# Kernel optimization log

Hardware: AMD Instinct MI355X
Metric: run time of the kernel (lower is better)

## Reference

```python
import jax, jax.numpy as jnp
import numpy as np

D_MODEL, JOINT_DIM, VOCAB = 512, 640, 1024
B, T, U = 4, 256, 64


def setup_inputs() -> dict:
    key = jax.random.key(0)
    ks = jax.random.split(key, 8)
    s_in = 1.0 / np.sqrt(D_MODEL)
    s_j = 1.0 / np.sqrt(JOINT_DIM)
    return {
        "enc": jax.random.normal(ks[0], (B, T, D_MODEL), jnp.float32),
        "pred": jax.random.normal(ks[1], (B, U, D_MODEL), jnp.float32),
        "enc_w": jax.random.uniform(ks[2], (JOINT_DIM, D_MODEL), jnp.float32, -s_in, s_in),
        "enc_b": jax.random.uniform(ks[3], (JOINT_DIM,), jnp.float32, -s_in, s_in),
        "pred_w": jax.random.uniform(ks[4], (JOINT_DIM, D_MODEL), jnp.float32, -s_in, s_in),
        "pred_b": jax.random.uniform(ks[5], (JOINT_DIM,), jnp.float32, -s_in, s_in),
        "out_w": jax.random.uniform(ks[6], (VOCAB, JOINT_DIM), jnp.float32, -s_j, s_j),
        "out_b": jax.random.uniform(ks[7], (VOCAB,), jnp.float32, -s_j, s_j),
    }


def reference(enc, pred, enc_w, enc_b, pred_w, pred_b, out_w, out_b):
    # project encoder (B,T,J) and predictor (B,U,J)
    e = jnp.einsum("btd,jd->btj", enc, enc_w) + enc_b
    p = jnp.einsum("bud,jd->buj", pred, pred_w) + pred_b
    # broadcast add over the (T,U) grid, tanh, then vocab projection
    z = jnp.tanh(e[:, :, None, :] + p[:, None, :, :])  # (B,T,U,J)
    logits = jnp.einsum("btuj,vj->btuv", z, out_w) + out_b  # (B,T,U,V)
    return logits
```

## Files before the change

kernel.cpp:

```cpp
#include <hip/hip_runtime.h>
#include <cstdint>
#include <cstddef>


typedef __attribute__((ext_vector_type(8))) __bf16 bf16x8;
typedef __attribute__((ext_vector_type(4))) float f32x4;

__device__ __forceinline__ int swz(int row, int kElem) {
  return (row << 6) + (kElem ^ ((row & 7) << 3));
}

__device__ __forceinline__ float fast_tanh(float x) {
  float e = __builtin_amdgcn_exp2f(x * 2.88539008177793f);
  return 1.0f - 2.0f * __builtin_amdgcn_rcpf(e + 1.0f);
}

__device__ __forceinline__ void gload_lds16(const void* g, void* l) {
  __builtin_amdgcn_global_load_lds(
      (const __attribute__((address_space(1))) void*)g,
      (__attribute__((address_space(3))) void*)l, 16, 0, 0);
}

__device__ void proj_tile(const float* __restrict__ A, const float* __restrict__ W,
                          const float* __restrict__ bias, __bf16* __restrict__ C,
                          int mt, int nt, __bf16* As, __bf16* Bs)
{
  const int tid  = threadIdx.x;
  const int r = tid & 127, half = tid >> 7;
  const int lane = tid & 63, wv = tid >> 6;
  const int wm = wv >> 1, wn = wv & 1;

  const float* arow = A + (size_t)(mt * 128 + r) * 512 + half * 32;
  const float* wrow = W + (size_t)(nt * 128 + r) * 512 + half * 32;

  f32x4 acc[4][4] = {};

  for (int k0 = 0; k0 < 512; k0 += 64) {
#pragma unroll
    for (int s = 0; s < 4; ++s) {
      f32x4 a0 = *(const f32x4*)(arow + k0 + s * 8);
      f32x4 a1 = *(const f32x4*)(arow + k0 + s * 8 + 4);
      f32x4 w0 = *(const f32x4*)(wrow + k0 + s * 8);
      f32x4 w1 = *(const f32x4*)(wrow + k0 + s * 8 + 4);
      bf16x8 za, zw;
#pragma unroll
      for (int j = 0; j < 4; ++j) {
        za[j] = (__bf16)a0[j]; za[4 + j] = (__bf16)a1[j];
        zw[j] = (__bf16)w0[j]; zw[4 + j] = (__bf16)w1[j];
      }
      const int kk = half * 32 + s * 8;
      *(bf16x8*)&As[swz(r, kk)] = za;
      *(bf16x8*)&Bs[swz(r, kk)] = zw;
    }
    __syncthreads();
#pragma unroll
    for (int kk = 0; kk < 2; ++kk) {
      bf16x8 af[4], bfr[4];
#pragma unroll
      for (int i = 0; i < 4; ++i) {
        af[i]  = *(const bf16x8*)&As[swz(wm * 64 + i * 16 + (lane & 15), kk * 32 + (lane >> 4) * 8)];
        bfr[i] = *(const bf16x8*)&Bs[swz(wn * 64 + i * 16 + (lane & 15), kk * 32 + (lane >> 4) * 8)];
      }
#pragma unroll
      for (int mi = 0; mi < 4; ++mi)
#pragma unroll
        for (int ni = 0; ni < 4; ++ni)
          acc[mi][ni] = __builtin_amdgcn_mfma_f32_16x16x32_bf16(af[mi], bfr[ni], acc[mi][ni], 0, 0, 0);
    }
    __syncthreads();
  }

  const int rowbase = mt * 128 + wm * 64;
  const int colbase = nt * 128 + wn * 64;
#pragma unroll
  for (int ni = 0; ni < 4; ++ni) {
    const int col = colbase + ni * 16 + (lane & 15);
    const float bb = bias[col];
#pragma unroll
    for (int mi = 0; mi < 4; ++mi) {
      const int row = rowbase + mi * 16 + (lane >> 4) * 4;
#pragma unroll
      for (int rg = 0; rg < 4; ++rg)
        C[(size_t)(row + rg) * 640 + col] = (__bf16)(acc[mi][ni][rg] + bb);
    }
  }
}

__global__ __launch_bounds__(256) void prep_kernel(
    const float* __restrict__ enc,  const float* __restrict__ enc_w,  const float* __restrict__ enc_b,
    const float* __restrict__ pred, const float* __restrict__ pred_w, const float* __restrict__ pred_b,
    const float* __restrict__ out_w,
    __bf16* __restrict__ E, __bf16* __restrict__ P, __bf16* __restrict__ Wb)
{
  __shared__ __align__(16) __bf16 As[128 * 64];
  __shared__ __align__(16) __bf16 Bs[128 * 64];
  const int bid = blockIdx.x;
  if (bid < 40) {
    proj_tile(enc, enc_w, enc_b, E, bid / 5, bid % 5, As, Bs);
  } else if (bid < 50) {
    proj_tile(pred, pred_w, pred_b, P, (bid - 40) / 5, (bid - 40) % 5, As, Bs);
  } else {
    const int gid = (bid - 50) * 256 + threadIdx.x;
    const int v  = gid / 80;
    const int j8 = gid % 80;
    f32x4 w0 = *(const f32x4*)(out_w + (size_t)v * 640 + j8 * 8);
    f32x4 w1 = *(const f32x4*)(out_w + (size_t)v * 640 + j8 * 8 + 4);
    bf16x8 z;
#pragma unroll
    for (int j = 0; j < 4; ++j) { z[j] = (__bf16)w0[j]; z[4 + j] = (__bf16)w1[j]; }
    const int nb = v >> 8, rr = v & 255;
    const int kb = j8 >> 3, kk = (j8 & 7) * 8;
    *(bf16x8*)(Wb + ((size_t)(nb * 10 + kb) << 14) + swz(rr, kk)) = z;
  }
}

__global__ __launch_bounds__(512, 4) void joiner_main(
    const __bf16* __restrict__ E, const __bf16* __restrict__ P,
    const __bf16* __restrict__ Wb, const float* __restrict__ outb,
    float* __restrict__ out)
{
  __shared__ __align__(16) __bf16 As[8192];
  __shared__ __align__(16) __bf16 Bs[2][16384];
  const int tid = threadIdx.x;
  const int nt = blockIdx.x & 3;
  const int mt = blockIdx.x >> 2;
  const int row0 = mt << 7;
  const int b  = row0 >> 14;
  const int t0 = (row0 >> 6) & 255;
  const int ar = tid & 127, h = tid >> 7;
  const int lane = tid & 63, wv = tid >> 6;
  const int wm = wv >> 2, wn = wv & 3;

  const __bf16* ep = E + (size_t)((b << 8) + t0 + (ar >> 6)) * 640 + h * 16;
  const __bf16* pp = P + (size_t)((b << 6) + (ar & 63)) * 640 + h * 16;
  const __bf16* wsrc = Wb + ((size_t)(nt * 10) << 14);

  f32x4 acc[4][4] = {};
  bf16x8 eA[2], pA[2];

  auto stageB = [&](int kt, __bf16* dst) {
#pragma unroll
    for (int c = 0; c < 4; ++c)
      gload_lds16(wsrc + ((size_t)kt << 14) + c * 4096 + wv * 512 + lane * 8,
                  dst + c * 4096 + wv * 512);
  };
  auto loadEP = [&](int k0) {
#pragma unroll
    for (int c = 0; c < 2; ++c) {
      eA[c] = *(const bf16x8*)(ep + k0 + c * 8);
      pA[c] = *(const bf16x8*)(pp + k0 + c * 8);
    }
  };
  auto writeA = [&]() {
#pragma unroll
    for (int c = 0; c < 2; ++c) {
      bf16x8 z;
#pragma unroll
      for (int j = 0; j < 8; ++j)
        z[j] = (__bf16)fast_tanh((float)eA[c][j] + (float)pA[c][j]);
      *(bf16x8*)&As[swz(ar, h * 16 + c * 8)] = z;
    }
  };
  auto compute = [&](const __bf16* Bsc) {
#pragma unroll
    for (int kk = 0; kk < 2; ++kk) {
      bf16x8 af[4], bfr[4];
#pragma unroll
      for (int i = 0; i < 4; ++i) {
        af[i]  = *(const bf16x8*)&As[swz(wm * 64 + i * 16 + (lane & 15), kk * 32 + (lane >> 4) * 8)];
        bfr[i] = *(const bf16x8*)&Bsc[swz(wn * 64 + i * 16 + (lane & 15), kk * 32 + (lane >> 4) * 8)];
      }
      asm volatile("s_waitcnt lgkmcnt(0)" ::: "memory");
      __builtin_amdgcn_sched_barrier(0);
      __builtin_amdgcn_s_setprio(1);
#pragma unroll
      for (int mi = 0; mi < 4; ++mi)
#pragma unroll
        for (int ni = 0; ni < 4; ++ni)
          acc[mi][ni] = __builtin_amdgcn_mfma_f32_16x16x32_bf16(af[mi], bfr[ni], acc[mi][ni], 0, 0, 0);
      __builtin_amdgcn_s_setprio(0);
    }
  };

  stageB(0, Bs[0]);
  loadEP(0);
  writeA();
  asm volatile("s_waitcnt vmcnt(0) lgkmcnt(0)" ::: "memory");
  __builtin_amdgcn_s_barrier();

  for (int kt = 0; kt < 9; ++kt) {
    const int cur = kt & 1;
    stageB(kt + 1, Bs[cur ^ 1]);
    loadEP((kt + 1) << 6);
    compute(Bs[cur]);
    __builtin_amdgcn_s_barrier();
    __builtin_amdgcn_sched_barrier(0);
    writeA();
    asm volatile("s_waitcnt lgkmcnt(0)" ::: "memory");
    __builtin_amdgcn_s_barrier();
  }
  compute(Bs[1]);

  const int rowbase = row0 + wm * 64;
  const int colbase = (nt << 8) + wn * 64;
#pragma unroll
  for (int ni = 0; ni < 4; ++ni) {
    const int col = colbase + ni * 16 + (lane & 15);
    const float bb = outb[col];
#pragma unroll
    for (int mi = 0; mi < 4; ++mi) {
      const int row = rowbase + mi * 16 + (lane >> 4) * 4;
#pragma unroll
      for (int rg = 0; rg < 4; ++rg)
        out[(size_t)(row + rg) * 1024 + col] = acc[mi][ni][rg] + bb;
    }
  }
}

extern "C" void kernel_launch(void* const* d_in, const int* in_sizes, int n_in,
                              void* d_out, int out_size, void* d_ws, size_t ws_size,
                              hipStream_t stream) {
  const float* enc    = (const float*)d_in[0];
  const float* pred   = (const float*)d_in[1];
  const float* enc_w  = (const float*)d_in[2];
  const float* enc_b  = (const float*)d_in[3];
  const float* pred_w = (const float*)d_in[4];
  const float* pred_b = (const float*)d_in[5];
  const float* out_w  = (const float*)d_in[6];
  const float* out_b  = (const float*)d_in[7];
  float* out = (float*)d_out;

  char* ws = (char*)d_ws;
  __bf16* E  = (__bf16*)(ws);
  __bf16* P  = (__bf16*)(ws + 1310720);
  __bf16* Wb = (__bf16*)(ws + 1638400);

  prep_kernel<<<dim3(370), dim3(256), 0, stream>>>(
      enc, enc_w, enc_b, pred, pred_w, pred_b, out_w, E, P, Wb);
  joiner_main<<<dim3(2048), dim3(512), 0, stream>>>(E, P, Wb, out_b, out);
}
```

Measured before the change: 172.8 us.

## Materialize tanh joint tensor then run plain tiled GEMM, fallback to fused

```diff
diff --git a/kernel.cpp b/kernel.cpp
--- a/kernel.cpp
+++ b/kernel.cpp
@@ -108,13 +108,102 @@
     bf16x8 z;
 #pragma unroll
     for (int j = 0; j < 4; ++j) { z[j] = (__bf16)w0[j]; z[4 + j] = (__bf16)w1[j]; }
-    const int nb = v >> 8, rr = v & 255;
+    const int nb = v >> 7, rr = v & 127;
     const int kb = j8 >> 3, kk = (j8 & 7) * 8;
-    *(bf16x8*)(Wb + ((size_t)(nb * 10 + kb) << 14) + swz(rr, kk)) = z;
-  }
-}
-
-__global__ __launch_bounds__(512, 4) void joiner_main(
+    *(bf16x8*)(Wb + ((size_t)(nb * 10 + kb) << 13) + swz(rr, kk)) = z;
+  }
+}
+
+__global__ __launch_bounds__(256) void zprod_kernel(
+    const __bf16* __restrict__ E, const __bf16* __restrict__ P,
+    __bf16* __restrict__ Z)
+{
+  const int bid = blockIdx.x;
+  const int mt = bid / 10, kt = bid % 10;
+  const int row0 = mt << 7;
+  const int b  = row0 >> 14;
+  const int t0 = (row0 >> 6) & 255;
+  __bf16* zdst = Z + ((size_t)bid << 13);
+  const int k0 = kt << 6;
+
+#pragma unroll
+  for (int c = 0; c < 4; ++c) {
+    const int o = c * 2048 + threadIdx.x * 8;
+    const int r = o >> 6;
+    const int k = (o & 63) ^ ((r & 7) << 3);
+    const __bf16* ep = E + (size_t)((b << 8) + t0 + (r >> 6)) * 640 + k0 + k;
+    const __bf16* pp = P + (size_t)((b << 6) + (r & 63)) * 640 + k0 + k;
+    bf16x8 e8 = *(const bf16x8*)ep;
+    bf16x8 p8 = *(const bf16x8*)pp;
+    bf16x8 z;
+#pragma unroll
+    for (int j = 0; j < 8; ++j)
+      z[j] = (__bf16)fast_tanh((float)e8[j] + (float)p8[j]);
+    *(bf16x8*)&zdst[o] = z;
+  }
+}
+
+__global__ __launch_bounds__(256) void joiner_mainz(
+    const __bf16* __restrict__ Z, const __bf16* __restrict__ Wb,
+    const float* __restrict__ outb, float* __restrict__ out)
+{
+  __shared__ __align__(16) __bf16 As[8192];
+  __shared__ __align__(16) __bf16 Bs[8192];
+  const int wg = blockIdx.x;
+  const int bid = (wg & 7) * 512 + (wg >> 3);
+  const int mt = bid >> 3, nt = bid & 7;
+  const int tid = threadIdx.x;
+  const int lane = tid & 63, wv = tid >> 6;
+  const int wm = wv >> 1, wn = wv & 1;
+
+  const __bf16* zsrc = Z  + ((size_t)(mt * 10) << 13);
+  const __bf16* wsrc = Wb + ((size_t)(nt * 10) << 13);
+
+  f32x4 acc[4][4] = {};
+
+  for (int kt = 0; kt < 10; ++kt) {
+    const size_t kb = (size_t)kt << 13;
+#pragma unroll
+    for (int c = 0; c < 4; ++c) {
+      const int off = c * 2048 + wv * 512;
+      gload_lds16(zsrc + kb + off + lane * 8, &As[off]);
+      gload_lds16(wsrc + kb + off + lane * 8, &Bs[off]);
+    }
+    __syncthreads();
+#pragma unroll
+    for (int kk = 0; kk < 2; ++kk) {
+      bf16x8 af[4], bfr[4];
+#pragma unroll
+      for (int i = 0; i < 4; ++i) {
+        af[i]  = *(const bf16x8*)&As[swz(wm * 64 + i * 16 + (lane & 15), kk * 32 + (lane >> 4) * 8)];
+        bfr[i] = *(const bf16x8*)&Bs[swz(wn * 64 + i * 16 + (lane & 15), kk * 32 + (lane >> 4) * 8)];
+      }
+#pragma unroll
+      for (int mi = 0; mi < 4; ++mi)
+#pragma unroll
+        for (int ni = 0; ni < 4; ++ni)
+          acc[mi][ni] = __builtin_amdgcn_mfma_f32_16x16x32_bf16(af[mi], bfr[ni], acc[mi][ni], 0, 0, 0);
+    }
+    __syncthreads();
+  }
+
+  const int rowbase = (mt << 7) + wm * 64;
+  const int colbase = (nt << 7) + wn * 64;
+#pragma unroll
+  for (int ni = 0; ni < 4; ++ni) {
+    const int col = colbase + ni * 16 + (lane & 15);
+    const float bb = outb[col];
+#pragma unroll
+    for (int mi = 0; mi < 4; ++mi) {
+      const int row = rowbase + mi * 16 + (lane >> 4) * 4;
+#pragma unroll
+      for (int rg = 0; rg < 4; ++rg)
+        out[(size_t)(row + rg) * 1024 + col] = acc[mi][ni][rg] + bb;
+    }
+  }
+}
+
+__global__ __launch_bounds__(512, 4) void joiner_fused(
     const __bf16* __restrict__ E, const __bf16* __restrict__ P,
     const __bf16* __restrict__ Wb, const float* __restrict__ outb,
     float* __restrict__ out)
@@ -133,16 +222,29 @@
 
   const __bf16* ep = E + (size_t)((b << 8) + t0 + (ar >> 6)) * 640 + h * 16;
   const __bf16* pp = P + (size_t)((b << 6) + (ar & 63)) * 640 + h * 16;
-  const __bf16* wsrc = Wb + ((size_t)(nt * 10) << 14);
 
   f32x4 acc[4][4] = {};
   bf16x8 eA[2], pA[2];
 
   auto stageB = [&](int kt, __bf16* dst) {
 #pragma unroll
-    for (int c = 0; c < 4; ++c)
-      gload_lds16(wsrc + ((size_t)kt << 14) + c * 4096 + wv * 512 + lane * 8,
-                  dst + c * 4096 + wv * 512);
+    for (int c = 0; c < 4; ++c) {
+      const int blk = nt * 2 + (c >> 1);
+      const int off = (c & 1) * 4096 + wv * 512;
+      gload_lds16(Wb + ((size_t)(blk * 10 + kt) << 13) + off + lane * 8,
+                  dst + c * 2048 * 2 - (c >> 1) * 8192 + ((c & 1) * 4096 + wv * 512) - ((c & 1) * 4096 + wv * 512) + (c * 4096 - (c >> 1) * 8192) * 0 + 0);
+    }
+  };
+  (void)stageB;
+
+  auto stageB2 = [&](int kt, __bf16* dst) {
+#pragma unroll
+    for (int c = 0; c < 4; ++c) {
+      const int blk = nt * 2 + (c >> 1);
+      const int inoff = (c & 1) * 4096 + wv * 512;
+      gload_lds16(Wb + ((size_t)(blk * 10 + kt) << 13) + inoff + lane * 8,
+                  dst + (c >> 1) * 8192 + inoff);
+    }
   };
   auto loadEP = [&](int k0) {
 #pragma unroll
@@ -182,7 +284,7 @@
     }
   };
 
-  stageB(0, Bs[0]);
+  stageB2(0, Bs[0]);
   loadEP(0);
   writeA();
   asm volatile("s_waitcnt vmcnt(0) lgkmcnt(0)" ::: "memory");
@@ -190,7 +292,7 @@
 
   for (int kt = 0; kt < 9; ++kt) {
     const int cur = kt & 1;
-    stageB(kt + 1, Bs[cur ^ 1]);
+    stageB2(kt + 1, Bs[cur ^ 1]);
     loadEP((kt + 1) << 6);
     compute(Bs[cur]);
     __builtin_amdgcn_s_barrier();
@@ -234,8 +336,15 @@
   __bf16* E  = (__bf16*)(ws);
   __bf16* P  = (__bf16*)(ws + 1310720);
   __bf16* Wb = (__bf16*)(ws + 1638400);
+  __bf16* Z  = (__bf16*)(ws + 2949120);
 
   prep_kernel<<<dim3(370), dim3(256), 0, stream>>>(
       enc, enc_w, enc_b, pred, pred_w, pred_b, out_w, E, P, Wb);
-  joiner_main<<<dim3(2048), dim3(512), 0, stream>>>(E, P, Wb, out_b, out);
-}
+
+  if (ws_size >= (size_t)86835200) {
+    zprod_kernel<<<dim3(5120), dim3(256), 0, stream>>>(E, P, Z);
+    joiner_mainz<<<dim3(4096), dim3(256), 0, stream>>>(Z, Wb, out_b, out);
+  } else {
+    joiner_fused<<<dim3(2048), dim3(512), 0, stream>>>(E, P, Wb, out_b, out);
+  }
+}
```

Result: no change. 171.7 us (-0.7%).
